# Performance work log

Measured on AMD Instinct MI355X. Metric: run time of the kernel, lower is better.

## Reference

```python
import jax, jax.numpy as jnp
import numpy as np

N_EMBD = 1024
VOCAB = 64
B, T = 8, 4096


def setup_inputs() -> dict:
    key = jax.random.key(0)
    ks = jax.random.split(key, 6)
    x = jax.random.normal(ks[0], (B, T, N_EMBD), dtype=jnp.float32)
    idx = jax.random.randint(ks[1], (B, T), 0, VOCAB, dtype=jnp.int64)
    emb_weight = jax.random.normal(ks[2], (VOCAB, N_EMBD), dtype=jnp.float32)
    head_weight = jax.random.normal(ks[3], (VOCAB, N_EMBD), dtype=jnp.float32)
    gate = jax.random.normal(ks[4], (1, 1, N_EMBD), dtype=jnp.float32) * 0.01
    soft_gate = jax.random.normal(ks[5], (1, 1, N_EMBD), dtype=jnp.float32) * 0.01
    return {"x": x, "idx": idx, "emb_weight": emb_weight,
            "head_weight": head_weight, "gate": gate, "soft_gate": soft_gate}


def reference(x, idx, emb_weight, head_weight, gate, soft_gate):
    # --- idx-gated codebook blend (idx from previous step's argmax, clamped >= 0) ---
    idx_c = jnp.clip(idx, 0, None)
    emb = emb_weight[idx_c]                                  # [B,T,D]
    g = jax.nn.sigmoid(x * gate).mean(axis=-1, keepdims=True)  # [B,T,1]
    x = x * (1.0 - g) + emb * g
    # (tmix/cmix are external and treated as identity here)
    # --- small-vocab head + softmax-weighted codebook lookup ---
    logits = jnp.einsum('btd,vd->btv', x, head_weight)        # [B,T,64]
    soft_prob = jax.nn.softmax(logits, axis=-1)
    soft_emb = jnp.einsum('btv,vd->btd', soft_prob, emb_weight)
    sg = jax.nn.sigmoid(x * soft_gate).mean(axis=-1, keepdims=True)
    x = x * (1.0 - sg) + soft_emb * sg
    # --- argmax indexing for next step ---
    new_idx = jnp.argmax(logits, axis=-1)                     # [B,T]
    return x, new_idx
```

## Files before the change

### kernel.cpp

```cpp
#include <hip/hip_runtime.h>
#include <hip/hip_bf16.h>


#define DIMS 1024
#define VOCAB 64
#define NTOK 32768
#define TTILE 16
#define TPB 512
#define IDX_OFF (NTOK * DIMS)
#define CAND_DELTA 1.25f

typedef __attribute__((ext_vector_type(8))) short short8;
typedef __attribute__((ext_vector_type(4))) float f32x4;

__device__ __forceinline__ float sigm(float z) {
    float zz = z * z;
    return fmaf(z, fmaf(zz, -(1.f / 48.f), 0.25f), 0.5f);
}
__device__ __forceinline__ unsigned short f2bf(float f) {
    __hip_bfloat16 h = __float2bfloat16(f);
    return *reinterpret_cast<unsigned short*>(&h);
}
__device__ __forceinline__ float bf2f(unsigned short u) {
    __hip_bfloat16 h = *reinterpret_cast<__hip_bfloat16*>(&u);
    return __bfloat162float(h);
}

__global__ void prep_weights(const float* __restrict__ head,
                             const float* __restrict__ emb,
                             __hip_bfloat16* __restrict__ headB,
                             __hip_bfloat16* __restrict__ embT) {
    int t = blockIdx.x * 256 + threadIdx.x;
    headB[t] = __float2bfloat16(head[t]);
    int d = t >> 6, v = t & 63;
    embT[t] = __float2bfloat16(emb[v * DIMS + d]);
}

__global__ __launch_bounds__(TPB) void fused_block(
    const float* __restrict__ x,
    const int* __restrict__ idx,
    const float* __restrict__ emb,
    const float* __restrict__ gate,
    const float* __restrict__ sgate,
    const float* __restrict__ headF,
    const __hip_bfloat16* __restrict__ headB,
    const __hip_bfloat16* __restrict__ embT,
    float* __restrict__ out)
{
    __shared__ __align__(16) __hip_bfloat16 sX1b[TTILE][1032];
    __shared__ __align__(16) float          sLogP[2][TTILE][68];
    __shared__ __align__(16) __hip_bfloat16 sP[TTILE][72];
    __shared__ float sSg[TTILE];

    const int tid  = threadIdx.x;
    const int tk   = tid >> 5;
    const int l32  = tid & 31;
    const long t0  = (long)blockIdx.x * TTILE;
    const long tok = t0 + tk;

    float4 xv[8];
    float gsum = 0.f;
    int ic = idx[tok]; if (ic < 0) ic = 0;
    const float4* xrow = (const float4*)(x + tok * DIMS);
    const float4* grow = (const float4*)gate;
    #pragma unroll
    for (int c = 0; c < 8; c++) {
        int f = l32 + c * 32;
        float4 v = xrow[f];
        float4 gv = grow[f];
        xv[c] = v;
        gsum += sigm(v.x * gv.x) + sigm(v.y * gv.y)
              + sigm(v.z * gv.z) + sigm(v.w * gv.w);
    }
    gsum += __shfl_xor(gsum, 1); gsum += __shfl_xor(gsum, 2);
    gsum += __shfl_xor(gsum, 4); gsum += __shfl_xor(gsum, 8);
    gsum += __shfl_xor(gsum, 16);
    const float g = gsum * (1.f / 1024.f);

    const float4* erow = (const float4*)(emb + (long)ic * DIMS);
    const float4* srow = (const float4*)sgate;
    float ssum = 0.f;
    #pragma unroll
    for (int c = 0; c < 8; c++) {
        int f = l32 + c * 32;
        float4 ev = erow[f];
        float4 sv = srow[f];
        float4 a;
        a.x = xv[c].x * (1.f - g) + ev.x * g;
        a.y = xv[c].y * (1.f - g) + ev.y * g;
        a.z = xv[c].z * (1.f - g) + ev.z * g;
        a.w = xv[c].w * (1.f - g) + ev.w * g;
        xv[c] = a;
        ssum += sigm(a.x * sv.x) + sigm(a.y * sv.y)
              + sigm(a.z * sv.z) + sigm(a.w * sv.w);
        ushort4 pk;
        pk.x = f2bf(a.x); pk.y = f2bf(a.y); pk.z = f2bf(a.z); pk.w = f2bf(a.w);
        *(ushort4*)&sX1b[tk][f * 4] = pk;
    }
    ssum += __shfl_xor(ssum, 1); ssum += __shfl_xor(ssum, 2);
    ssum += __shfl_xor(ssum, 4); ssum += __shfl_xor(ssum, 8);
    ssum += __shfl_xor(ssum, 16);
    if (l32 == 0) sSg[tk] = ssum * (1.f / 1024.f);
    __syncthreads();

    const int w    = tid >> 6;
    const int lane = tid & 63;
    const int quad = lane >> 4, l16 = lane & 15;
    const int nt   = w & 3;
    const int kh   = w >> 2;
    {
        f32x4 acc = {0.f, 0.f, 0.f, 0.f};
        const __hip_bfloat16* hrow = headB + (long)(nt * 16 + l16) * DIMS + kh * 512 + quad * 8;
        #pragma unroll 4
        for (int k0 = 0; k0 < 512; k0 += 32) {
            short8 a = *(const short8*)&sX1b[l16][kh * 512 + k0 + quad * 8];
            short8 b = *(const short8*)(hrow + k0);
            acc = __builtin_amdgcn_mfma_f32_16x16x32_bf16(a, b, acc, 0, 0, 0);
        }
        #pragma unroll
        for (int i = 0; i < 4; i++)
            sLogP[kh][quad * 4 + i][nt * 16 + l16] = acc[i];
    }
    __syncthreads();

    unsigned long long candA, candB;
    {
        float lA = sLogP[0][2 * w][lane]     + sLogP[1][2 * w][lane];
        float lB = sLogP[0][2 * w + 1][lane] + sLogP[1][2 * w + 1][lane];
        float mA = lA, mB = lB;
        #pragma unroll
        for (int k = 1; k < 64; k <<= 1) {
            mA = fmaxf(mA, __shfl_xor(mA, k));
            mB = fmaxf(mB, __shfl_xor(mB, k));
        }
        float eA = __expf(lA - mA), eB = __expf(lB - mB);
        float sA = eA, sB = eB;
        #pragma unroll
        for (int k = 1; k < 64; k <<= 1) {
            sA += __shfl_xor(sA, k);
            sB += __shfl_xor(sB, k);
        }
        sP[2 * w][lane]     = __float2bfloat16(eA * __builtin_amdgcn_rcpf(sA));
        sP[2 * w + 1][lane] = __float2bfloat16(eB * __builtin_amdgcn_rcpf(sB));
        candA = __ballot(lA >= mA - CAND_DELTA);
        candB = __ballot(lB >= mB - CAND_DELTA);
    }
    __syncthreads();

    {
        float sgv[4];
        #pragma unroll
        for (int r = 0; r < 4; r++) sgv[r] = sSg[quad * 4 + r];
        #pragma unroll 1
        for (int i = 0; i < 8; i++) {
            int n0 = (i * 8 + w) * 16;
            f32x4 acc = {0.f, 0.f, 0.f, 0.f};
            #pragma unroll
            for (int k0 = 0; k0 < VOCAB; k0 += 32) {
                short8 a = *(const short8*)&sP[l16][k0 + quad * 8];
                short8 b = *(const short8*)(embT + (long)(n0 + l16) * VOCAB + k0 + quad * 8);
                acc = __builtin_amdgcn_mfma_f32_16x16x32_bf16(a, b, acc, 0, 0, 0);
            }
            #pragma unroll
            for (int r = 0; r < 4; r++) {
                int m = quad * 4 + r;
                int n = n0 + l16;
                float x1f = bf2f(*(const unsigned short*)&sX1b[m][n]);
                out[(t0 + m) * (long)DIMS + n] = x1f * (1.f - sgv[r]) + acc[r] * sgv[r];
            }
        }
    }

    {
        unsigned long long cm = ((lane >> 5) & 1) ? candB : candA;
        int bi;
        if (__popcll(cm) == 1) {
            bi = __ffsll(cm) - 1;
        } else {
            float bv = -3.4e38f; bi = 0;
            while (cm) {
                int v = __ffsll(cm) - 1;
                cm &= cm - 1;
                const float4* hr = (const float4*)(headF + (long)v * DIMS);
                float p = 0.f;
                #pragma unroll
                for (int c = 0; c < 8; c++) {
                    float4 hv = hr[l32 + c * 32];
                    p = fmaf(xv[c].x, hv.x, p); p = fmaf(xv[c].y, hv.y, p);
                    p = fmaf(xv[c].z, hv.z, p); p = fmaf(xv[c].w, hv.w, p);
                }
                p += __shfl_xor(p, 1); p += __shfl_xor(p, 2);
                p += __shfl_xor(p, 4); p += __shfl_xor(p, 8);
                p += __shfl_xor(p, 16);
                if (p > bv) { bv = p; bi = v; }
            }
        }
        if (l32 == 0) out[IDX_OFF + tok] = (float)bi;
    }
}

extern "C" void kernel_launch(void* const* d_in, const int* in_sizes, int n_in,
                              void* d_out, int out_size, void* d_ws, size_t ws_size,
                              hipStream_t stream) {
    const float* xp    = (const float*)d_in[0];
    const int*   idxp  = (const int*)d_in[1];
    const float* embp  = (const float*)d_in[2];
    const float* headp = (const float*)d_in[3];
    const float* gp    = (const float*)d_in[4];
    const float* sgp   = (const float*)d_in[5];
    float*       outp  = (float*)d_out;

    __hip_bfloat16* headB = (__hip_bfloat16*)d_ws;
    __hip_bfloat16* embT  = (__hip_bfloat16*)((char*)d_ws + 131072);

    prep_weights<<<dim3(256), dim3(256), 0, stream>>>(headp, embp, headB, embT);
    fused_block<<<dim3(NTOK / TTILE), dim3(TPB), 0, stream>>>(
        xp, idxp, embp, gp, sgp, headp, headB, embT, outp);
}
```

Measured before the change: 285.9 us.

## Precompute emb·head table and compute logits from raw x, blending linearly

Uses linearity of the head projection: logits of the blended x equal (1-g)*x·head + g*emb[idx]·head, with the second term read from a 64x64 table precomputed in the prep kernel. The logit MFMA can then start on raw x, and the gate reduction is computed after issuing it instead of before. The blended x is rewritten to shared memory after the softmax stage for the output pass. This adds a table computation in the prep kernel and an extra shared-memory write of the tile. Rounding changes because x is cast to bf16 before blending, which may affect argmax candidates.

New measurement: 324.1 us. 13.4% more time.

```diff
diff --git a/kernel.cpp b/kernel.cpp
--- a/kernel.cpp
+++ b/kernel.cpp
@@ -29,11 +29,25 @@
 __global__ void prep_weights(const float* __restrict__ head,
                              const float* __restrict__ emb,
                              __hip_bfloat16* __restrict__ headB,
-                             __hip_bfloat16* __restrict__ embT) {
+                             __hip_bfloat16* __restrict__ embT,
+                             float* __restrict__ ehF) {
     int t = blockIdx.x * 256 + threadIdx.x;
     headB[t] = __float2bfloat16(head[t]);
     int d = t >> 6, v = t & 63;
     embT[t] = __float2bfloat16(emb[v * DIMS + d]);
+    if (t < VOCAB * VOCAB) {
+        int u = t >> 6, vv = t & 63;
+        const float4* er = (const float4*)(emb + (long)u * DIMS);
+        const float4* hr = (const float4*)(head + (long)vv * DIMS);
+        float s = 0.f;
+        #pragma unroll 4
+        for (int k = 0; k < 256; k++) {
+            float4 a = er[k], b = hr[k];
+            s = fmaf(a.x, b.x, s); s = fmaf(a.y, b.y, s);
+            s = fmaf(a.z, b.z, s); s = fmaf(a.w, b.w, s);
+        }
+        ehF[t] = s;
+    }
 }
 
 __global__ __launch_bounds__(TPB) void fused_block(
@@ -45,6 +59,7 @@
     const float* __restrict__ headF,
     const __hip_bfloat16* __restrict__ headB,
     const __hip_bfloat16* __restrict__ embT,
+    const float* __restrict__ ehF,
     float* __restrict__ out)
 {
     __shared__ __align__(16) __hip_bfloat16 sX1b[TTILE][1032];
@@ -58,49 +73,20 @@
     const long t0  = (long)blockIdx.x * TTILE;
     const long tok = t0 + tk;
 
-    float4 xv[8];
-    float gsum = 0.f;
+    float4 xv[8], ev[8];
     int ic = idx[tok]; if (ic < 0) ic = 0;
+    const float4* erow = (const float4*)(emb + (long)ic * DIMS);
     const float4* xrow = (const float4*)(x + tok * DIMS);
-    const float4* grow = (const float4*)gate;
     #pragma unroll
     for (int c = 0; c < 8; c++) {
         int f = l32 + c * 32;
+        ev[c] = erow[f];
         float4 v = xrow[f];
-        float4 gv = grow[f];
         xv[c] = v;
-        gsum += sigm(v.x * gv.x) + sigm(v.y * gv.y)
-              + sigm(v.z * gv.z) + sigm(v.w * gv.w);
-    }
-    gsum += __shfl_xor(gsum, 1); gsum += __shfl_xor(gsum, 2);
-    gsum += __shfl_xor(gsum, 4); gsum += __shfl_xor(gsum, 8);
-    gsum += __shfl_xor(gsum, 16);
-    const float g = gsum * (1.f / 1024.f);
-
-    const float4* erow = (const float4*)(emb + (long)ic * DIMS);
-    const float4* srow = (const float4*)sgate;
-    float ssum = 0.f;
-    #pragma unroll
-    for (int c = 0; c < 8; c++) {
-        int f = l32 + c * 32;
-        float4 ev = erow[f];
-        float4 sv = srow[f];
-        float4 a;
-        a.x = xv[c].x * (1.f - g) + ev.x * g;
-        a.y = xv[c].y * (1.f - g) + ev.y * g;
-        a.z = xv[c].z * (1.f - g) + ev.z * g;
-        a.w = xv[c].w * (1.f - g) + ev.w * g;
-        xv[c] = a;
-        ssum += sigm(a.x * sv.x) + sigm(a.y * sv.y)
-              + sigm(a.z * sv.z) + sigm(a.w * sv.w);
         ushort4 pk;
-        pk.x = f2bf(a.x); pk.y = f2bf(a.y); pk.z = f2bf(a.z); pk.w = f2bf(a.w);
+        pk.x = f2bf(v.x); pk.y = f2bf(v.y); pk.z = f2bf(v.z); pk.w = f2bf(v.w);
         *(ushort4*)&sX1b[tk][f * 4] = pk;
     }
-    ssum += __shfl_xor(ssum, 1); ssum += __shfl_xor(ssum, 2);
-    ssum += __shfl_xor(ssum, 4); ssum += __shfl_xor(ssum, 8);
-    ssum += __shfl_xor(ssum, 16);
-    if (l32 == 0) sSg[tk] = ssum * (1.f / 1024.f);
     __syncthreads();
 
     const int w    = tid >> 6;
@@ -121,12 +107,55 @@
         for (int i = 0; i < 4; i++)
             sLogP[kh][quad * 4 + i][nt * 16 + l16] = acc[i];
     }
+
+    float g;
+    {
+        const float4* grow = (const float4*)gate;
+        float gsum = 0.f;
+        #pragma unroll
+        for (int c = 0; c < 8; c++) {
+            int f = l32 + c * 32;
+            float4 gv = grow[f];
+            gsum += sigm(xv[c].x * gv.x) + sigm(xv[c].y * gv.y)
+                  + sigm(xv[c].z * gv.z) + sigm(xv[c].w * gv.w);
+        }
+        gsum += __shfl_xor(gsum, 1); gsum += __shfl_xor(gsum, 2);
+        gsum += __shfl_xor(gsum, 4); gsum += __shfl_xor(gsum, 8);
+        gsum += __shfl_xor(gsum, 16);
+        g = gsum * (1.f / 1024.f);
+
+        const float4* srow = (const float4*)sgate;
+        float ssum = 0.f;
+        #pragma unroll
+        for (int c = 0; c < 8; c++) {
+            int f = l32 + c * 32;
+            float4 sv = srow[f];
+            float4 a;
+            a.x = xv[c].x * (1.f - g) + ev[c].x * g;
+            a.y = xv[c].y * (1.f - g) + ev[c].y * g;
+            a.z = xv[c].z * (1.f - g) + ev[c].z * g;
+            a.w = xv[c].w * (1.f - g) + ev[c].w * g;
+            xv[c] = a;
+            ssum += sigm(a.x * sv.x) + sigm(a.y * sv.y)
+                  + sigm(a.z * sv.z) + sigm(a.w * sv.w);
+        }
+        ssum += __shfl_xor(ssum, 1); ssum += __shfl_xor(ssum, 2);
+        ssum += __shfl_xor(ssum, 4); ssum += __shfl_xor(ssum, 8);
+        ssum += __shfl_xor(ssum, 16);
+        if (l32 == 0) sSg[tk] = ssum * (1.f / 1024.f);
+    }
     __syncthreads();
 
     unsigned long long candA, candB;
     {
-        float lA = sLogP[0][2 * w][lane]     + sLogP[1][2 * w][lane];
-        float lB = sLogP[0][2 * w + 1][lane] + sLogP[1][2 * w + 1][lane];
+        int   icA = __shfl(ic, 0),  icB = __shfl(ic, 32);
+        float gA  = __shfl(g, 0),   gB  = __shfl(g, 32);
+        float ehA = ehF[icA * VOCAB + lane];
+        float ehB = ehF[icB * VOCAB + lane];
+        float xlA = sLogP[0][2 * w][lane]     + sLogP[1][2 * w][lane];
+        float xlB = sLogP[0][2 * w + 1][lane] + sLogP[1][2 * w + 1][lane];
+        float lA = (1.f - gA) * xlA + gA * ehA;
+        float lB = (1.f - gB) * xlB + gB * ehB;
         float mA = lA, mB = lB;
         #pragma unroll
         for (int k = 1; k < 64; k <<= 1) {
@@ -144,6 +173,15 @@
         sP[2 * w + 1][lane] = __float2bfloat16(eB * __builtin_amdgcn_rcpf(sB));
         candA = __ballot(lA >= mA - CAND_DELTA);
         candB = __ballot(lB >= mB - CAND_DELTA);
+    }
+
+    #pragma unroll
+    for (int c = 0; c < 8; c++) {
+        int f = l32 + c * 32;
+        ushort4 pk;
+        pk.x = f2bf(xv[c].x); pk.y = f2bf(xv[c].y);
+        pk.z = f2bf(xv[c].z); pk.w = f2bf(xv[c].w);
+        *(ushort4*)&sX1b[tk][f * 4] = pk;
     }
     __syncthreads();
 
@@ -212,8 +250,9 @@
 
     __hip_bfloat16* headB = (__hip_bfloat16*)d_ws;
     __hip_bfloat16* embT  = (__hip_bfloat16*)((char*)d_ws + 131072);
-
-    prep_weights<<<dim3(256), dim3(256), 0, stream>>>(headp, embp, headB, embT);
+    float*          ehF   = (float*)((char*)d_ws + 262144);
+
+    prep_weights<<<dim3(256), dim3(256), 0, stream>>>(headp, embp, headB, embT, ehF);
     fused_block<<<dim3(NTOK / TTILE), dim3(TPB), 0, stream>>>(
-        xp, idxp, embp, gp, sgp, headp, headB, embT, outp);
-}
+        xp, idxp, embp, gp, sgp, headp, headB, embT, ehF, outp);
+}
```
